# Kernel tuning notes

Hardware: AMD Instinct MI355X
Metric: run time of the kernel (lower is better)

The kernel has to match this reference:

```python
import jax, jax.numpy as jnp
import numpy as np

N_NODES = 100000
N_EDGES = 1600000
D_IN = 128
D_HID = 128
N_CLASS = 10
N_GRAPHS = 512
BN_EPS = 1e-5


def setup_inputs() -> dict:
    key = jax.random.key(0)
    ks = jax.random.split(key, 12)
    x = jax.random.normal(ks[0], (N_NODES, D_IN), dtype=jnp.float32)
    edge_index = jax.random.randint(ks[1], (2, N_EDGES), 0, N_NODES, dtype=jnp.int32)
    idx = jnp.sort(jax.random.randint(ks[2], (N_NODES,), 0, N_GRAPHS, dtype=jnp.int32))
    s = 1.0 / np.sqrt(D_HID)
    W1 = jax.random.uniform(ks[3], (D_IN, D_HID), minval=-s, maxval=s, dtype=jnp.float32)
    b1 = jnp.zeros((D_HID,), jnp.float32)
    W2 = jax.random.uniform(ks[4], (D_HID, D_HID), minval=-s, maxval=s, dtype=jnp.float32)
    b2 = jnp.zeros((D_HID,), jnp.float32)
    W3 = jax.random.uniform(ks[5], (D_HID, D_HID), minval=-s, maxval=s, dtype=jnp.float32)
    b3 = jnp.zeros((D_HID,), jnp.float32)
    W4 = jax.random.uniform(ks[6], (D_HID, N_CLASS), minval=-s, maxval=s, dtype=jnp.float32)
    b4 = jnp.zeros((N_CLASS,), jnp.float32)
    gamma = jnp.ones((D_HID,), jnp.float32)
    beta = jnp.zeros((D_HID,), jnp.float32)
    return {"x": x, "edge_index": edge_index, "idx": idx,
            "W1": W1, "b1": b1, "W2": W2, "b2": b2,
            "W3": W3, "b3": b3, "W4": W4, "b4": b4,
            "gamma": gamma, "beta": beta}


def _agg(h, src, dst):
    # (adj + I) @ h : sum of neighbor features plus self-loop
    return jax.ops.segment_sum(h[src], dst, num_segments=N_NODES) + h


def reference(x, edge_index, idx, W1, b1, W2, b2, W3, b3, W4, b4, gamma, beta):
    src, dst = edge_index[0], edge_index[1]
    z1 = jax.nn.relu(_agg(x, src, dst) @ W1 + b1)          # [N, H] (dropout = identity, eval)
    h = _agg(z1, src, dst) @ W2 + b2                        # [N, H]
    pooled = jax.ops.segment_sum(h, idx, num_segments=N_GRAPHS)  # [G, H] scatter-add readout
    # BatchNorm1d over graph (batch) dimension, training-mode batch stats
    mean = jnp.mean(pooled, axis=0)
    var = jnp.var(pooled, axis=0)
    out = (pooled - mean) * jax.lax.rsqrt(var + BN_EPS) * gamma + beta
    zg = jax.nn.relu(out @ W3 + b3)
    logits = zg @ W4 + b4                                   # [G, C]
    return jax.nn.log_softmax(logits, axis=1)
```

## Files before the change

kernel.cpp:

```cpp
#include <hip/hip_runtime.h>
#include <hip/hip_fp16.h>
#include <math.h>

#define NN 100000
#define NE 1600000
#define DH 128
#define NG 512
#define NC 10
#define NSEG 8
#define SEGN 12500
#define CHE 8192
#define NCH 196
#define MAXDEG 48
#define WPITCH 136

#define NB_HIST (NCH * NSEG)
#define NB_CNT  98
#define NB_GEMM ((NN + 63) / 64)

typedef __attribute__((ext_vector_type(8))) _Float16 f16x8;
typedef __attribute__((ext_vector_type(4))) float f32x4;


__global__ __launch_bounds__(256, 3) void k_build(
    const int* __restrict__ dst, const int* __restrict__ src,
    int* __restrict__ counts, int* __restrict__ csr,
    const int* __restrict__ gidx, int* __restrict__ cnt,
    const float* __restrict__ A, const float* __restrict__ W,
    __half* __restrict__ out) {
    int b = blockIdx.x;
    int t = threadIdx.x;
    if (b < NB_HIST) {
        int seg = b & 7;
        int chunk = b >> 3;
        int lo = seg * SEGN, hi = lo + SEGN;
        int e0 = chunk * CHE;
        int e1 = e0 + CHE < NE ? e0 + CHE : NE;
        for (int e = e0 + t * 4; e < e1; e += 1024) {
            int4 d4 = *(const int4*)(dst + e);
            bool i0 = d4.x >= lo && d4.x < hi;
            bool i1 = d4.y >= lo && d4.y < hi;
            bool i2 = d4.z >= lo && d4.z < hi;
            bool i3 = d4.w >= lo && d4.w < hi;
            int4 s4 = {0, 0, 0, 0};
            if (i0 | i1 | i2 | i3) s4 = *(const int4*)(src + e);
            if (i0) {
                int p = atomicAdd(&counts[d4.x], 1);
                if (p < MAXDEG) csr[d4.x * MAXDEG + p] = s4.x;
            }
            if (i1) {
                int p = atomicAdd(&counts[d4.y], 1);
                if (p < MAXDEG) csr[d4.y * MAXDEG + p] = s4.y;
            }
            if (i2) {
                int p = atomicAdd(&counts[d4.z], 1);
                if (p < MAXDEG) csr[d4.z * MAXDEG + p] = s4.z;
            }
            if (i3) {
                int p = atomicAdd(&counts[d4.w], 1);
                if (p < MAXDEG) csr[d4.w * MAXDEG + p] = s4.w;
            }
        }
    } else if (b < NB_HIST + NB_CNT) {
        int cb = b - NB_HIST;
        int n0 = cb * 1024 + t * 4;
        if (n0 >= NN) return;
        int g = gidx[n0];
        int run = 1;
        for (int j = 1; j < 4; ++j) {
            int n = n0 + j;
            if (n < NN) {
                int gg = gidx[n];
                if (gg == g) {
                    run++;
                } else {
                    atomicAdd(&cnt[g], run);
                    g = gg;
                    run = 1;
                }
            }
        }
        atomicAdd(&cnt[g], run);
    } else {
        __shared__ _Float16 sWT[DH * WPITCH];
        __shared__ __align__(16) _Float16 sOut[4][16][DH];
        int gb = b - (NB_HIST + NB_CNT);
        int wv = t >> 6;
        int lane = t & 63;
        for (int i = t; i < DH * DH; i += 256) {
            int k = i >> 7, n = i & 127;
            sWT[n * WPITCH + k] = (_Float16)W[i];
        }
        __syncthreads();

        int m = lane & 15;
        int quad = lane >> 4;
        int node0 = gb * 64 + wv * 16;
        int nodeA = node0 + m;
        if (nodeA >= NN) nodeA = NN - 1;
        const float* arow = A + (size_t)nodeA * DH;

        f16x8 afrag[4];
#pragma unroll
        for (int kt = 0; kt < 4; ++kt) {
            int k0 = kt * 32 + quad * 8;
            float4 u0 = *(const float4*)(arow + k0);
            float4 u1 = *(const float4*)(arow + k0 + 4);
            afrag[kt][0] = (_Float16)u0.x; afrag[kt][1] = (_Float16)u0.y;
            afrag[kt][2] = (_Float16)u0.z; afrag[kt][3] = (_Float16)u0.w;
            afrag[kt][4] = (_Float16)u1.x; afrag[kt][5] = (_Float16)u1.y;
            afrag[kt][6] = (_Float16)u1.z; afrag[kt][7] = (_Float16)u1.w;
        }

#pragma unroll
        for (int ct = 0; ct < 8; ++ct) {
            f32x4 acc = {0.f, 0.f, 0.f, 0.f};
            int n = ct * 16 + m;
#pragma unroll
            for (int kt = 0; kt < 4; ++kt) {
                int k0 = kt * 32 + quad * 8;
                f16x8 bfrag = *(const f16x8*)&sWT[n * WPITCH + k0];
                acc = __builtin_amdgcn_mfma_f32_16x16x32_f16(afrag[kt], bfrag, acc, 0, 0, 0);
            }
#pragma unroll
            for (int r = 0; r < 4; ++r)
                sOut[wv][quad * 4 + r][ct * 16 + m] = (_Float16)acc[r];
        }
        __syncthreads();

        const uint4* so = (const uint4*)&sOut[wv][0][0];
        for (int i = lane; i < 256; i += 64) {
            int row = i >> 4;
            int node = node0 + row;
            if (node < NN) ((uint4*)out)[(size_t)node * 16 + (i & 15)] = so[i];
        }
    }
}


__device__ __forceinline__ void acc8(float* a, const uint4& v, float m) {
    float2 f;
    f = __half22float2(*(const __half2*)&v.x); a[0] = fmaf(m, f.x, a[0]); a[1] = fmaf(m, f.y, a[1]);
    f = __half22float2(*(const __half2*)&v.y); a[2] = fmaf(m, f.x, a[2]); a[3] = fmaf(m, f.y, a[3]);
    f = __half22float2(*(const __half2*)&v.z); a[4] = fmaf(m, f.x, a[4]); a[5] = fmaf(m, f.y, a[5]);
    f = __half22float2(*(const __half2*)&v.w); a[6] = fmaf(m, f.x, a[6]); a[7] = fmaf(m, f.y, a[7]);
}


__global__ __launch_bounds__(256, 4) void k_agg_h(
    const __half* __restrict__ in, const int* __restrict__ counts,
    const int* __restrict__ csr, const float* __restrict__ bias,
    __half* __restrict__ outA) {
    int t = threadIdx.x;
    int lane = t & 15;
    int node = blockIdx.x * 16 + (t >> 4);
    const uint4* in4 = (const uint4*)in;
    float a[8];
#pragma unroll
    for (int j = 0; j < 8; ++j) a[j] = 0.f;
    uint4 sv = in4[(size_t)node * 16 + lane];
    acc8(a, sv, 1.f);
    int e0 = node * MAXDEG;
    int deg = counts[node];
    deg = deg < MAXDEG ? deg : MAXDEG;
    int e1 = e0 + deg;
    int elast = e1 - 1;
    for (int e = e0; e < e1; e += 8) {
        int idx[8];
        float m[8];
#pragma unroll
        for (int i = 0; i < 8; ++i) {
            int ei = e + i;
            int ec = ei < elast ? ei : elast;
            idx[i] = csr[ec];
            m[i] = (ei < e1) ? 1.f : 0.f;
        }
        uint4 v[8];
#pragma unroll
        for (int i = 0; i < 8; ++i) v[i] = in4[(size_t)idx[i] * 16 + lane];
#pragma unroll
        for (int i = 0; i < 8; ++i) acc8(a, v[i], m[i]);
    }
    float4 b0 = ((const float4*)bias)[lane * 2];
    float4 b1v = ((const float4*)bias)[lane * 2 + 1];
    a[0] = fmaxf(a[0] + b0.x, 0.f);  a[1] = fmaxf(a[1] + b0.y, 0.f);
    a[2] = fmaxf(a[2] + b0.z, 0.f);  a[3] = fmaxf(a[3] + b0.w, 0.f);
    a[4] = fmaxf(a[4] + b1v.x, 0.f); a[5] = fmaxf(a[5] + b1v.y, 0.f);
    a[6] = fmaxf(a[6] + b1v.z, 0.f); a[7] = fmaxf(a[7] + b1v.w, 0.f);
    uint4 o;
    *(__half2*)&o.x = __floats2half2_rn(a[0], a[1]);
    *(__half2*)&o.y = __floats2half2_rn(a[2], a[3]);
    *(__half2*)&o.z = __floats2half2_rn(a[4], a[5]);
    *(__half2*)&o.w = __floats2half2_rn(a[6], a[7]);
    ((uint4*)outA)[(size_t)node * 16 + lane] = o;
}


__global__ __launch_bounds__(256, 4) void k_agg_pool_h(
    const __half* __restrict__ in, const int* __restrict__ counts,
    const int* __restrict__ csr, const int* __restrict__ gidx,
    float* __restrict__ pp8) {
    __shared__ __align__(16) float sA[16][DH];
    int t = threadIdx.x;
    int lane = t & 15;
    int p = t >> 4;
    int node0 = blockIdx.x * 16;
    int node = node0 + p;
    const uint4* in4 = (const uint4*)in;
    float a[8];
#pragma unroll
    for (int j = 0; j < 8; ++j) a[j] = 0.f;
    uint4 sv = in4[(size_t)node * 16 + lane];
    acc8(a, sv, 1.f);
    int e0 = node * MAXDEG;
    int deg = counts[node];
    deg = deg < MAXDEG ? deg : MAXDEG;
    int e1 = e0 + deg;
    int elast = e1 - 1;
    for (int e = e0; e < e1; e += 8) {
        int idx[8];
        float m[8];
#pragma unroll
        for (int i = 0; i < 8; ++i) {
            int ei = e + i;
            int ec = ei < elast ? ei : elast;
            idx[i] = csr[ec];
            m[i] = (ei < e1) ? 1.f : 0.f;
        }
        uint4 v[8];
#pragma unroll
        for (int i = 0; i < 8; ++i) v[i] = in4[(size_t)idx[i] * 16 + lane];
#pragma unroll
        for (int i = 0; i < 8; ++i) acc8(a, v[i], m[i]);
    }
    float4* row = (float4*)&sA[p][lane * 8];
    row[0] = make_float4(a[0], a[1], a[2], a[3]);
    row[1] = make_float4(a[4], a[5], a[6], a[7]);
    __syncthreads();
    if (t < DH) {
        float* pp = pp8 + (size_t)(blockIdx.x & 7) * NG * DH;
        int gprev = gidx[node0];
        float run = 0.f;
        for (int q = 0; q < 16; ++q) {
            int g = gidx[node0 + q];
            if (g != gprev) {
                atomicAdd(&pp[gprev * DH + t], run);
                run = 0.f;
                gprev = g;
            }
            run += sA[q][t];
        }
        atomicAdd(&pp[gprev * DH + t], run);
    }
}


__device__ __forceinline__ void fma4(float4& acc, float s, const float4& wv) {
    acc.x = fmaf(s, wv.x, acc.x);
    acc.y = fmaf(s, wv.y, acc.y);
    acc.z = fmaf(s, wv.z, acc.z);
    acc.w = fmaf(s, wv.w, acc.w);
}


__global__ __launch_bounds__(256, 2) void k_pool_mm(
    const float* __restrict__ pp8, const float* __restrict__ W,
    const float* __restrict__ bias, const int* __restrict__ cnt,
    float* __restrict__ pooled) {
    __shared__ __align__(16) float sW[DH * DH];
    __shared__ __align__(16) float sA[32 * DH];
    int t = threadIdx.x;
    int g0 = blockIdx.x * 32;
    {
        const float4* W4g = (const float4*)W;
        float4* sW4 = (float4*)sW;
        for (int i = t; i < DH * DH / 4; i += 256) sW4[i] = W4g[i];
        const float4* P4 = (const float4*)pp8;
        float4* sA4 = (float4*)sA;
        for (int i = t; i < 32 * DH / 4; i += 256) {
            float4 s;
            s.x = 0.f; s.y = 0.f; s.z = 0.f; s.w = 0.f;
#pragma unroll
            for (int c = 0; c < NSEG; ++c) {
                float4 v = P4[(size_t)c * NG * DH / 4 + (size_t)g0 * DH / 4 + i];
                s.x += v.x; s.y += v.y; s.z += v.z; s.w += v.w;
            }
            sA4[i] = s;
        }
    }
    __syncthreads();

    int c4 = t & 31;
    int n0 = (t >> 5) * 4;
    const float4* sA4 = (const float4*)sA;
    const float4* sW4 = (const float4*)sW;
    float4 acc0, acc1, acc2, acc3;
    acc0.x = acc0.y = acc0.z = acc0.w = 0.f;
    acc1 = acc0; acc2 = acc0; acc3 = acc0;

#pragma unroll 2
    for (int kc = 0; kc < DH / 4; ++kc) {
        float4 a0 = sA4[(n0 + 0) * 32 + kc];
        float4 a1 = sA4[(n0 + 1) * 32 + kc];
        float4 a2 = sA4[(n0 + 2) * 32 + kc];
        float4 a3 = sA4[(n0 + 3) * 32 + kc];
        float4 w0 = sW4[(4 * kc + 0) * 32 + c4];
        float4 w1 = sW4[(4 * kc + 1) * 32 + c4];
        float4 w2 = sW4[(4 * kc + 2) * 32 + c4];
        float4 w3 = sW4[(4 * kc + 3) * 32 + c4];
        fma4(acc0, a0.x, w0); fma4(acc0, a0.y, w1); fma4(acc0, a0.z, w2); fma4(acc0, a0.w, w3);
        fma4(acc1, a1.x, w0); fma4(acc1, a1.y, w1); fma4(acc1, a1.z, w2); fma4(acc1, a1.w, w3);
        fma4(acc2, a2.x, w0); fma4(acc2, a2.y, w1); fma4(acc2, a2.z, w2); fma4(acc2, a2.w, w3);
        fma4(acc3, a3.x, w0); fma4(acc3, a3.y, w1); fma4(acc3, a3.z, w2); fma4(acc3, a3.w, w3);
    }

    float4 b2v = ((const float4*)bias)[c4];
    float c0 = (float)cnt[g0 + n0 + 0];
    float c1 = (float)cnt[g0 + n0 + 1];
    float c2 = (float)cnt[g0 + n0 + 2];
    float c3 = (float)cnt[g0 + n0 + 3];
    fma4(acc0, c0, b2v);
    fma4(acc1, c1, b2v);
    fma4(acc2, c2, b2v);
    fma4(acc3, c3, b2v);

    float4* out4 = (float4*)pooled;
    out4[(size_t)(g0 + n0 + 0) * 32 + c4] = acc0;
    out4[(size_t)(g0 + n0 + 1) * 32 + c4] = acc1;
    out4[(size_t)(g0 + n0 + 2) * 32 + c4] = acc2;
    out4[(size_t)(g0 + n0 + 3) * 32 + c4] = acc3;
}


__global__ void k_bnstats(const float* __restrict__ pooled, float* __restrict__ mean,
                          float* __restrict__ rstd) {
    int c = blockIdx.x;
    int l = threadIdx.x;
    float s = 0.f, s2 = 0.f;
    for (int g = l; g < NG; g += 64) {
        float v = pooled[g * DH + c];
        s += v;
        s2 += v * v;
    }
#pragma unroll
    for (int off = 32; off > 0; off >>= 1) {
        s += __shfl_down(s, off, 64);
        s2 += __shfl_down(s2, off, 64);
    }
    if (l == 0) {
        float m = s * (1.f / NG);
        float var = s2 * (1.f / NG) - m * m;
        mean[c] = m;
        rstd[c] = rsqrtf(var + 1e-5f);
    }
}


__global__ __launch_bounds__(128) void k_tail(
    const float* __restrict__ pooled, const float* __restrict__ mean,
    const float* __restrict__ rstd, const float* __restrict__ gamma,
    const float* __restrict__ beta, const float* __restrict__ W3,
    const float* __restrict__ b3, const float* __restrict__ W4,
    const float* __restrict__ b4, float* __restrict__ out) {
    __shared__ __align__(16) float sW[DH * DH];
    __shared__ float sg[DH];
    __shared__ float sz[DH];
    __shared__ float slog[NC];
    __shared__ float slse;
    int g = blockIdx.x, t = threadIdx.x;
    {
        const float4* W34 = (const float4*)W3;
        float4* sW4 = (float4*)sW;
        for (int i = t; i < DH * DH / 4; i += 128) sW4[i] = W34[i];
    }
    float v = pooled[g * DH + t];
    v = (v - mean[t]) * rstd[t] * gamma[t] + beta[t];
    sg[t] = v;
    __syncthreads();
    float acc = b3[t];
#pragma unroll 4
    for (int k = 0; k < DH; ++k) acc = fmaf(sg[k], sW[k * DH + t], acc);
    sz[t] = fmaxf(acc, 0.f);
    __syncthreads();
    if (t < NC) {
        float a = b4[t];
        for (int k = 0; k < DH; ++k) a = fmaf(sz[k], W4[k * NC + t], a);
        slog[t] = a;
    }
    __syncthreads();
    if (t == 0) {
        float mx = slog[0];
        for (int j = 1; j < NC; ++j) mx = fmaxf(mx, slog[j]);
        float se = 0.f;
        for (int j = 0; j < NC; ++j) se += expf(slog[j] - mx);
        slse = mx + logf(se);
    }
    __syncthreads();
    if (t < NC) out[g * NC + t] = slog[t] - slse;
}


extern "C" void kernel_launch(void* const* d_in, const int* in_sizes, int n_in,
                              void* d_out, int out_size, void* d_ws, size_t ws_size,
                              hipStream_t stream) {
    const float* x = (const float*)d_in[0];
    const int* ei = (const int*)d_in[1];
    const int* src = ei;
    const int* dst = ei + NE;
    const int* gidx = (const int*)d_in[2];
    const float* W1 = (const float*)d_in[3];
    const float* b1 = (const float*)d_in[4];
    const float* W2 = (const float*)d_in[5];
    const float* b2 = (const float*)d_in[6];
    const float* W3 = (const float*)d_in[7];
    const float* b3 = (const float*)d_in[8];
    const float* W4 = (const float*)d_in[9];
    const float* b4 = (const float*)d_in[10];
    const float* gamma = (const float*)d_in[11];
    const float* beta = (const float*)d_in[12];
    float* out = (float*)d_out;

    char* w = (char*)d_ws;
    auto take = [&](size_t bytes) {
        char* p = w;
        w += (bytes + 255) & ~size_t(255);
        return p;
    };
    int* counts = (int*)take((size_t)NN * 4);
    int* cnt = (int*)take((size_t)NG * 4);
    float* pp8 = (float*)take((size_t)NSEG * NG * DH * 4);
    size_t zero_bytes = (size_t)((char*)(pp8 + (size_t)NSEG * NG * DH) - (char*)counts);
    int* csr = (int*)take((size_t)NN * MAXDEG * 4);
    __half* y = (__half*)take((size_t)NN * DH * 2);
    __half* z1 = (__half*)take((size_t)NN * DH * 2);
    float* pooled = (float*)take((size_t)NG * DH * 4);
    float* meanb = (float*)take(DH * 4);
    float* rstdb = (float*)take(DH * 4);

    hipMemsetAsync(counts, 0, zero_bytes, stream);

    k_build<<<NB_HIST + NB_CNT + NB_GEMM, 256, 0, stream>>>(
        dst, src, counts, csr, gidx, cnt, x, W1, y);

    k_agg_h<<<NN / 16, 256, 0, stream>>>(y, counts, csr, b1, z1);

    k_agg_pool_h<<<NN / 16, 256, 0, stream>>>(z1, counts, csr, gidx, pp8);
    k_pool_mm<<<NG / 32, 256, 0, stream>>>(pp8, W2, b2, cnt, pooled);

    k_bnstats<<<DH, 64, 0, stream>>>(pooled, meanb, rstdb);
    k_tail<<<NG, 128, 0, stream>>>(pooled, meanb, rstdb, gamma, beta, W3, b3, W4, b4, out);
}
```

Baseline: 360.9 us.

## Use nontemporal loads/stores, split full/tail edge loops, raise agg occupancy

Streaming loads of edge arrays, CSR indices and the dense input now use nontemporal loads, and the fp16 outputs use nontemporal stores, so they do not pollute the cache that holds the gathered feature rows. The aggregation loops are split into a full-chunk loop without masking and a single masked tail chunk. Gather addresses use 32-bit byte offsets, and launch bounds for the aggregation kernels rise from 4 to 6 blocks per SM. The higher occupancy target may force register spills, and nontemporal stores of outputs that the next kernel reads may lose L2 reuse.

```diff
diff --git a/kernel.cpp b/kernel.cpp
--- a/kernel.cpp
+++ b/kernel.cpp
@@ -20,6 +20,8 @@
 
 typedef __attribute__((ext_vector_type(8))) _Float16 f16x8;
 typedef __attribute__((ext_vector_type(4))) float f32x4;
+typedef __attribute__((ext_vector_type(4))) int i32x4;
+typedef __attribute__((ext_vector_type(4))) unsigned int u32x4;
 
 
 __global__ __launch_bounds__(256, 3) void k_build(
@@ -37,13 +39,14 @@
         int e0 = chunk * CHE;
         int e1 = e0 + CHE < NE ? e0 + CHE : NE;
         for (int e = e0 + t * 4; e < e1; e += 1024) {
-            int4 d4 = *(const int4*)(dst + e);
+            i32x4 d4 = __builtin_nontemporal_load((const i32x4*)(dst + e));
             bool i0 = d4.x >= lo && d4.x < hi;
             bool i1 = d4.y >= lo && d4.y < hi;
             bool i2 = d4.z >= lo && d4.z < hi;
             bool i3 = d4.w >= lo && d4.w < hi;
-            int4 s4 = {0, 0, 0, 0};
-            if (i0 | i1 | i2 | i3) s4 = *(const int4*)(src + e);
+            i32x4 s4 = {0, 0, 0, 0};
+            if (i0 | i1 | i2 | i3)
+                s4 = __builtin_nontemporal_load((const i32x4*)(src + e));
             if (i0) {
                 int p = atomicAdd(&counts[d4.x], 1);
                 if (p < MAXDEG) csr[d4.x * MAXDEG + p] = s4.x;
@@ -104,8 +107,8 @@
 #pragma unroll
         for (int kt = 0; kt < 4; ++kt) {
             int k0 = kt * 32 + quad * 8;
-            float4 u0 = *(const float4*)(arow + k0);
-            float4 u1 = *(const float4*)(arow + k0 + 4);
+            f32x4 u0 = __builtin_nontemporal_load((const f32x4*)(arow + k0));
+            f32x4 u1 = __builtin_nontemporal_load((const f32x4*)(arow + k0 + 4));
             afrag[kt][0] = (_Float16)u0.x; afrag[kt][1] = (_Float16)u0.y;
             afrag[kt][2] = (_Float16)u0.z; afrag[kt][3] = (_Float16)u0.w;
             afrag[kt][4] = (_Float16)u1.x; afrag[kt][5] = (_Float16)u1.y;
@@ -132,7 +135,11 @@
         for (int i = lane; i < 256; i += 64) {
             int row = i >> 4;
             int node = node0 + row;
-            if (node < NN) ((uint4*)out)[(size_t)node * 16 + (i & 15)] = so[i];
+            if (node < NN) {
+                uint4 val = so[i];
+                __builtin_nontemporal_store(*(const u32x4*)&val,
+                                            (u32x4*)out + (size_t)node * 16 + (i & 15));
+            }
         }
     }
 }
@@ -147,37 +154,52 @@
 }
 
 
-__global__ __launch_bounds__(256, 4) void k_agg_h(
+__global__ __launch_bounds__(256, 6) void k_agg_h(
     const __half* __restrict__ in, const int* __restrict__ counts,
     const int* __restrict__ csr, const float* __restrict__ bias,
     __half* __restrict__ outA) {
     int t = threadIdx.x;
     int lane = t & 15;
     int node = blockIdx.x * 16 + (t >> 4);
-    const uint4* in4 = (const uint4*)in;
+    const char* inb = (const char*)in;
+    unsigned lb = (unsigned)lane * 16u;
     float a[8];
 #pragma unroll
     for (int j = 0; j < 8; ++j) a[j] = 0.f;
-    uint4 sv = in4[(size_t)node * 16 + lane];
+    uint4 sv = *(const uint4*)(inb + ((unsigned)node * 256u + lb));
     acc8(a, sv, 1.f);
     int e0 = node * MAXDEG;
     int deg = counts[node];
     deg = deg < MAXDEG ? deg : MAXDEG;
     int e1 = e0 + deg;
-    int elast = e1 - 1;
-    for (int e = e0; e < e1; e += 8) {
+    int e = e0;
+    int efull = e0 + (deg & ~7);
+    for (; e < efull; e += 8) {
+        int idx[8];
+#pragma unroll
+        for (int i = 0; i < 8; ++i) idx[i] = __builtin_nontemporal_load(csr + e + i);
+        uint4 v[8];
+#pragma unroll
+        for (int i = 0; i < 8; ++i)
+            v[i] = *(const uint4*)(inb + ((unsigned)idx[i] * 256u + lb));
+#pragma unroll
+        for (int i = 0; i < 8; ++i) acc8(a, v[i], 1.f);
+    }
+    if (e < e1) {
+        int elast = e1 - 1;
         int idx[8];
         float m[8];
 #pragma unroll
         for (int i = 0; i < 8; ++i) {
             int ei = e + i;
             int ec = ei < elast ? ei : elast;
-            idx[i] = csr[ec];
+            idx[i] = __builtin_nontemporal_load(csr + ec);
             m[i] = (ei < e1) ? 1.f : 0.f;
         }
         uint4 v[8];
 #pragma unroll
-        for (int i = 0; i < 8; ++i) v[i] = in4[(size_t)idx[i] * 16 + lane];
+        for (int i = 0; i < 8; ++i)
+            v[i] = *(const uint4*)(inb + ((unsigned)idx[i] * 256u + lb));
 #pragma unroll
         for (int i = 0; i < 8; ++i) acc8(a, v[i], m[i]);
     }
@@ -192,11 +214,12 @@
     *(__half2*)&o.y = __floats2half2_rn(a[2], a[3]);
     *(__half2*)&o.z = __floats2half2_rn(a[4], a[5]);
     *(__half2*)&o.w = __floats2half2_rn(a[6], a[7]);
-    ((uint4*)outA)[(size_t)node * 16 + lane] = o;
-}
-
-
-__global__ __launch_bounds__(256, 4) void k_agg_pool_h(
+    __builtin_nontemporal_store(*(const u32x4*)&o,
+                                (u32x4*)outA + (size_t)node * 16 + lane);
+}
+
+
+__global__ __launch_bounds__(256, 6) void k_agg_pool_h(
     const __half* __restrict__ in, const int* __restrict__ counts,
     const int* __restrict__ csr, const int* __restrict__ gidx,
     float* __restrict__ pp8) {
@@ -206,30 +229,45 @@
     int p = t >> 4;
     int node0 = blockIdx.x * 16;
     int node = node0 + p;
-    const uint4* in4 = (const uint4*)in;
+    const char* inb = (const char*)in;
+    unsigned lb = (unsigned)lane * 16u;
     float a[8];
 #pragma unroll
     for (int j = 0; j < 8; ++j) a[j] = 0.f;
-    uint4 sv = in4[(size_t)node * 16 + lane];
+    uint4 sv = *(const uint4*)(inb + ((unsigned)node * 256u + lb));
     acc8(a, sv, 1.f);
     int e0 = node * MAXDEG;
     int deg = counts[node];
     deg = deg < MAXDEG ? deg : MAXDEG;
     int e1 = e0 + deg;
-    int elast = e1 - 1;
-    for (int e = e0; e < e1; e += 8) {
+    int e = e0;
+    int efull = e0 + (deg & ~7);
+    for (; e < efull; e += 8) {
+        int idx[8];
+#pragma unroll
+        for (int i = 0; i < 8; ++i) idx[i] = __builtin_nontemporal_load(csr + e + i);
+        uint4 v[8];
+#pragma unroll
+        for (int i = 0; i < 8; ++i)
+            v[i] = *(const uint4*)(inb + ((unsigned)idx[i] * 256u + lb));
+#pragma unroll
+        for (int i = 0; i < 8; ++i) acc8(a, v[i], 1.f);
+    }
+    if (e < e1) {
+        int elast = e1 - 1;
         int idx[8];
         float m[8];
 #pragma unroll
         for (int i = 0; i < 8; ++i) {
             int ei = e + i;
             int ec = ei < elast ? ei : elast;
-            idx[i] = csr[ec];
+            idx[i] = __builtin_nontemporal_load(csr + ec);
             m[i] = (ei < e1) ? 1.f : 0.f;
         }
         uint4 v[8];
 #pragma unroll
-        for (int i = 0; i < 8; ++i) v[i] = in4[(size_t)idx[i] * 16 + lane];
+        for (int i = 0; i < 8; ++i)
+            v[i] = *(const uint4*)(inb + ((unsigned)idx[i] * 256u + lb));
 #pragma unroll
         for (int i = 0; i < 8; ++i) acc8(a, v[i], m[i]);
     }
```

Measured after the change: 393.7 us. 1.09x slower.
